# Kernel optimization log

Measured on AMD Instinct MI355X. Metric: run time of the kernel, lower is better.

The kernel has to match this reference:

```python
import jax, jax.numpy as jnp
import numpy as np

N_BUILD = 200000
N_COMM = 10000
E_BUILD = 1200000
E_COMM = 160000
D_B = 64    # building feature dim
D_C = 32    # community feature dim
H = 64      # hidden dim (comm embedding)
D_FUSE = D_B + H  # 128
N_CLS = 2


def gcn(x, src, dst, W, b):
    """PyG-style GCNConv with self-loops and symmetric normalization.
    out_i = sum_{j->i} h_j / sqrt(deg_j * deg_i) + h_i / deg_i + b, h = x @ W.
    deg counts in-edges plus the self-loop."""
    n = x.shape[0]
    h = x @ W                                   # [n, out]
    deg = jnp.ones((n,), x.dtype).at[dst].add(1.0)
    norm = jax.lax.rsqrt(deg)
    msg = h[src] * (norm[src] * norm[dst])[:, None]          # gather + edge weight
    agg = jax.ops.segment_sum(msg, dst, num_segments=n)      # scatter-add
    return agg + h * (1.0 / deg)[:, None] + b


def setup_inputs():
    key = jax.random.key(0)
    ks = jax.random.split(key, 24)
    f32 = jnp.float32

    def glorot(k, shape):
        scale = np.sqrt(2.0 / (shape[0] + shape[1])).astype(np.float32)
        return jax.random.normal(k, shape, dtype=f32) * scale

    inp = {
        "building_features": jax.random.normal(ks[0], (N_BUILD, D_B), dtype=f32),
        "community_features": jax.random.normal(ks[1], (N_COMM, D_C), dtype=f32),
        # GCN weights: comm 32->64->64, attention 128->2, building 128->128->64->2
        "W_c1": glorot(ks[2], (D_C, H)),   "b_c1": jnp.zeros((H,), f32),
        "W_c2": glorot(ks[3], (H, H)),     "b_c2": jnp.zeros((H,), f32),
        "W_att": glorot(ks[4], (D_FUSE, 2)), "b_att": jnp.zeros((2,), f32),
        "W_b1": glorot(ks[5], (D_FUSE, D_FUSE)), "b_b1": jnp.zeros((D_FUSE,), f32),
        "W_b2": glorot(ks[6], (D_FUSE, H)),       "b_b2": jnp.zeros((H,), f32),
        "W_b3": glorot(ks[7], (H, N_CLS)),         "b_b3": jnp.zeros((N_CLS,), f32),
        # edge lists (int) and index maps
        "b_src": jax.random.randint(ks[8], (E_BUILD,), 0, N_BUILD, dtype=jnp.int32),
        "b_dst": jax.random.randint(ks[9], (E_BUILD,), 0, N_BUILD, dtype=jnp.int32),
        "c_src": jax.random.randint(ks[10], (E_COMM,), 0, N_COMM, dtype=jnp.int32),
        "c_dst": jax.random.randint(ks[11], (E_COMM,), 0, N_COMM, dtype=jnp.int32),
        "building_to_comm_mapping": jax.random.randint(ks[12], (N_BUILD,), 0, N_COMM, dtype=jnp.int32),
        # Batch.from_data_list ordering: here identity permutation of buildings
        "local_to_global": jnp.arange(N_BUILD, dtype=jnp.int32),
    }
    return inp


def reference(building_features, community_features,
              W_c1, b_c1, W_c2, b_c2, W_att, b_att,
              W_b1, b_b1, W_b2, b_b2, W_b3, b_b3,
              b_src, b_dst, c_src, c_dst,
              building_to_comm_mapping, local_to_global):
    # Community GNN (dropout is identity in eval)
    comm_x = jax.nn.relu(gcn(community_features, c_src, c_dst, W_c1, b_c1))
    comm_x = jax.nn.relu(gcn(comm_x, c_src, c_dst, W_c2, b_c2))

    # Irregular gather: per-building community embedding
    building_comm = comm_x[building_to_comm_mapping]          # [N_build, H]

    # Feature attention: softmax gate over the two modalities
    logits = jnp.concatenate([building_features, building_comm], axis=1) @ W_att + b_att
    a = jax.nn.softmax(logits, axis=1)                        # [N_build, 2]
    fused = jnp.concatenate([building_features * a[:, 0:1],
                             building_comm * a[:, 1:2]], axis=1)  # [N_build, 128]

    # Batched building GNN over disjoint per-community subgraphs
    local_x = fused[local_to_global]
    x = jax.nn.relu(gcn(local_x, b_src, b_dst, W_b1, b_b1))
    x = jax.nn.relu(gcn(x, b_src, b_dst, W_b2, b_b2))
    x = gcn(x, b_src, b_dst, W_b3, b_b3)                      # [N_build, 2]

    # Scatter back to global order, then log-softmax
    combined = jnp.zeros((building_features.shape[0], N_CLS), x.dtype)
    combined = combined.at[local_to_global].set(x)
    return jax.nn.log_softmax(combined, axis=1)
```

## Files before the change

### kernel.cpp

```cpp
#include <hip/hip_runtime.h>
#include <hip/hip_bf16.h>
#include <math.h>

#define N_BUILD 200000
#define N_COMM  10000
#define E_BUILD 1200000
#define E_COMM  160000
#define NB_B 196
#define NB_C 10
#define CHUNK 2048
#define CB_B ((E_BUILD + CHUNK - 1) / CHUNK)
#define CB_C ((E_COMM  + CHUNK - 1) / CHUNK)

typedef __bf16 bf16x8 __attribute__((ext_vector_type(8)));
typedef float  f32x4  __attribute__((ext_vector_type(4)));

__device__ __forceinline__ unsigned short f2b(float f) {
    unsigned int u = __builtin_bit_cast(unsigned int, f);
    u += 0x7fffu + ((u >> 16) & 1u);
    return (unsigned short)(u >> 16);
}
__device__ __forceinline__ float b2f(unsigned short h) {
    unsigned int u = ((unsigned int)h) << 16;
    return __builtin_bit_cast(float, u);
}
__device__ __forceinline__ unsigned int pk2(float a, float b) {
    return (unsigned int)f2b(a) | ((unsigned int)f2b(b) << 16);
}
__device__ __forceinline__ void up8(uint4 v, float* r) {
    r[0] = b2f((unsigned short)v.x); r[1] = b2f((unsigned short)(v.x >> 16));
    r[2] = b2f((unsigned short)v.y); r[3] = b2f((unsigned short)(v.y >> 16));
    r[4] = b2f((unsigned short)v.z); r[5] = b2f((unsigned short)(v.z >> 16));
    r[6] = b2f((unsigned short)v.w); r[7] = b2f((unsigned short)(v.w >> 16));
}

#define INIT_TOT (N_BUILD + N_COMM + 2 * N_BUILD + N_COMM * 32 + 2048 + 4096 + 16384 + 8192)
__global__ __launch_bounds__(256) void init_k(int* cnt_b, int* cnt_c, float* out,
                                              const float* __restrict__ cF, unsigned short* __restrict__ cFb,
                                              const float* __restrict__ W_c1, unsigned short* __restrict__ Wt_c1,
                                              const float* __restrict__ W_c2, unsigned short* __restrict__ Wt_c2,
                                              const float* __restrict__ W_b1, unsigned short* __restrict__ Wt_b1,
                                              const float* __restrict__ W_b2, unsigned short* __restrict__ Wt_b2) {
    int i = blockIdx.x * blockDim.x + threadIdx.x;
    if (i < N_BUILD) { cnt_b[i] = 0; return; }
    i -= N_BUILD;
    if (i < N_COMM) { cnt_c[i] = 0; return; }
    i -= N_COMM;
    if (i < 2 * N_BUILD) { out[i] = -0.69314718056f; return; }
    i -= 2 * N_BUILD;
    if (i < N_COMM * 32) { cFb[i] = f2b(cF[i]); return; }
    i -= N_COMM * 32;
    if (i < 2048) { Wt_c1[(i % 64) * 32 + i / 64] = f2b(W_c1[i]); return; }
    i -= 2048;
    if (i < 4096) { Wt_c2[(i % 64) * 64 + i / 64] = f2b(W_c2[i]); return; }
    i -= 4096;
    if (i < 16384) { Wt_b1[(i % 128) * 128 + i / 128] = f2b(W_b1[i]); return; }
    i -= 16384;
    if (i < 8192) { Wt_b2[(i % 64) * 128 + i / 64] = f2b(W_b2[i]); }
}


__global__ __launch_bounds__(256) void hist2_k(int* cnt_b, const int* __restrict__ b_dst,
                                               int* cnt_c, const int* __restrict__ c_dst) {
    int i = blockIdx.x * blockDim.x + threadIdx.x;
    if (i < E_BUILD) atomicAdd(&cnt_b[b_dst[i]], 1);
    else if (i < E_BUILD + E_COMM) atomicAdd(&cnt_c[c_dst[i - E_BUILD]], 1);
}

__global__ __launch_bounds__(256) void scan1m_k(const int* __restrict__ cnt_b, int* __restrict__ ex_b, int* __restrict__ bs_b,
                                                const int* __restrict__ cnt_c, int* __restrict__ ex_c, int* __restrict__ bs_c) {
    __shared__ int sdata[256];
    const int tid = threadIdx.x;
    const int* cnt; int* ex; int* bs; int n, blk;
    if ((int)blockIdx.x < NB_B) { cnt = cnt_b; ex = ex_b; bs = bs_b; n = N_BUILD; blk = blockIdx.x; }
    else                        { cnt = cnt_c; ex = ex_c; bs = bs_c; n = N_COMM;  blk = blockIdx.x - NB_B; }
    const int base = blk * 1024 + tid * 4;
    int v[4]; int s = 0;
#pragma unroll
    for (int j = 0; j < 4; ++j) { v[j] = (base + j < n) ? cnt[base + j] : 0; s += v[j]; }
    sdata[tid] = s; __syncthreads();
    for (int off = 1; off < 256; off <<= 1) {
        int t = (tid >= off) ? sdata[tid - off] : 0;
        __syncthreads();
        sdata[tid] += t;
        __syncthreads();
    }
    if (tid == 255) bs[blk] = sdata[255];
    int run = sdata[tid] - s;
#pragma unroll
    for (int j = 0; j < 4; ++j) { if (base + j < n) ex[base + j] = run; run += v[j]; }
}

__global__ __launch_bounds__(256) void scan2m_k(int* bs_b, int* bs_c) {
    __shared__ int sdata[256];
    int* bs = (blockIdx.x == 0) ? bs_b : bs_c;
    int nb  = (blockIdx.x == 0) ? NB_B : NB_C;
    const int tid = threadIdx.x;
    int v = (tid < nb) ? bs[tid] : 0;
    sdata[tid] = v; __syncthreads();
    for (int off = 1; off < 256; off <<= 1) {
        int t = (tid >= off) ? sdata[tid - off] : 0;
        __syncthreads();
        sdata[tid] += t;
        __syncthreads();
    }
    if (tid < nb) bs[tid] = sdata[tid] - v;
}

__global__ __launch_bounds__(256) void finalizem_k(const int* __restrict__ cnt_b, int* rp_b, const int* __restrict__ bo_b,
                                                   int* cur_b, float* di_b,
                                                   const int* __restrict__ cnt_c, int* rp_c, const int* __restrict__ bo_c,
                                                   int* cur_c, float* di_c) {
    int i = blockIdx.x * blockDim.x + threadIdx.x;
    if (i < N_BUILD) {
        int cc = cnt_b[i];
        int r = rp_b[i] + bo_b[i >> 10];
        rp_b[i] = r; cur_b[i] = r; di_b[i] = 1.0f / (float)(cc + 1);
        if (i == 0) { rp_b[N_BUILD] = E_BUILD; rp_c[N_COMM] = E_COMM; }
    } else if (i < N_BUILD + N_COMM) {
        int ic = i - N_BUILD;
        int cc = cnt_c[ic];
        int r = rp_c[ic] + bo_c[ic >> 10];
        rp_c[ic] = r; cur_c[ic] = r; di_c[ic] = 1.0f / (float)(cc + 1);
    }
}

template<int NDIV>
__device__ __forceinline__ void scatter_part(const int* __restrict__ src, const int* __restrict__ dst,
                                             int* cur, const float* __restrict__ di,
                                             int2* __restrict__ cse, int E, int cid, int x) {
    int base = cid * CHUNK + threadIdx.x;
#pragma unroll
    for (int j = 0; j < CHUNK / 256; ++j, base += 256) {
        if (base < E) {
            int d = dst[base];
            if ((unsigned)d / (unsigned)NDIV == (unsigned)x) {
                int s = src[base];
                int pos = atomicAdd(&cur[d], 1);
                cse[pos] = make_int2(s, __float_as_int(sqrtf(di[s] * di[d])));
            }
        }
    }
}

__global__ __launch_bounds__(256) void csr_scatterp_k(const int* __restrict__ b_src, const int* __restrict__ b_dst,
                                                      int* cur_b, const float* __restrict__ di_b, int2* __restrict__ cse_b,
                                                      const int* __restrict__ c_src, const int* __restrict__ c_dst,
                                                      int* cur_c, const float* __restrict__ di_c, int2* __restrict__ cse_c) {
    int bid = blockIdx.x;
    if (bid < 8 * CB_B) {
        scatter_part<N_BUILD / 8>(b_src, b_dst, cur_b, di_b, cse_b, E_BUILD, bid >> 3, bid & 7);
    } else {
        bid -= 8 * CB_B;
        scatter_part<N_COMM / 8>(c_src, c_dst, cur_c, di_c, cse_c, E_COMM, bid >> 3, bid & 7);
    }
}

template<int K, int N, bool GUARD>
__global__ __launch_bounds__(256) void gemm_mfma_k(const unsigned short* __restrict__ X,
                                                   const unsigned short* __restrict__ Wt,
                                                   unsigned short* __restrict__ H, int M) {
    constexpr int GPR = K / 8;
    __shared__ unsigned short sA[64 * K];
    __shared__ unsigned short sB[N * K];
    const int tid  = threadIdx.x;
    const int row0 = blockIdx.x * 64;

    for (int idx = tid; idx < 64 * GPR; idx += 256) {
        int r = idx / GPR, g = idx % GPR;
        uint4 v = make_uint4(0u, 0u, 0u, 0u);
        if (!GUARD || row0 + r < M)
            v = *(const uint4*)&X[(size_t)(row0 + r) * K + g * 8];
        int gs = g ^ (r & (GPR - 1));
        *(uint4*)&sA[r * K + gs * 8] = v;
    }
    for (int idx = tid; idx < N * GPR; idx += 256) {
        int r = idx / GPR, g = idx % GPR;
        uint4 v = *(const uint4*)&Wt[(size_t)r * K + g * 8];
        int gs = g ^ (r & (GPR - 1));
        *(uint4*)&sB[r * K + gs * 8] = v;
    }
    __syncthreads();

    const int wave = tid >> 6, lane = tid & 63;
    const int rA = wave * 16 + (lane & 15);
    const int kg = lane >> 4;

    f32x4 zero = {0.f, 0.f, 0.f, 0.f};
    f32x4 acc[N / 16];
#pragma unroll
    for (int t = 0; t < N / 16; ++t) acc[t] = zero;

#pragma unroll
    for (int ks = 0; ks < K / 32; ++ks) {
        int gA = (ks * 4 + kg) ^ (rA & (GPR - 1));
        bf16x8 a = *(const bf16x8*)&sA[rA * K + gA * 8];
#pragma unroll
        for (int t = 0; t < N / 16; ++t) {
            int rB = t * 16 + (lane & 15);
            int gB = (ks * 4 + kg) ^ (rB & (GPR - 1));
            bf16x8 b = *(const bf16x8*)&sB[rB * K + gB * 8];
            acc[t] = __builtin_amdgcn_mfma_f32_16x16x32_bf16(a, b, acc[t], 0, 0, 0);
        }
    }

    const int crow = wave * 16 + (lane >> 4) * 4;
    const int ccol = lane & 15;
#pragma unroll
    for (int t = 0; t < N / 16; ++t) {
#pragma unroll
        for (int j = 0; j < 4; ++j) {
            int r = row0 + crow + j;
            if (!GUARD || r < M)
                H[(size_t)r * N + t * 16 + ccol] = f2b(acc[t][j]);
        }
    }
}

__global__ __launch_bounds__(256) void attscal_k(const float* __restrict__ bF,
                                                 const unsigned short* __restrict__ cx,
                                                 const int* __restrict__ map,
                                                 const int* __restrict__ l2g,
                                                 const float* __restrict__ Watt,
                                                 const float* __restrict__ batt,
                                                 unsigned short* __restrict__ bFl,
                                                 float2* __restrict__ afus,
                                                 int* __restrict__ mbl, int n) {
    __shared__ float sW0[128], sW1[128];
    if (threadIdx.x < 128) {
        sW0[threadIdx.x] = Watt[threadIdx.x * 2 + 0];
        sW1[threadIdx.x] = Watt[threadIdx.x * 2 + 1];
    }
    __syncthreads();
    int gid = blockIdx.x * blockDim.x + threadIdx.x;
    int i = gid >> 3, j = gid & 7;
    if (i >= n) return;
    int g = l2g[i];
    int mg = map[g];
    const float* f1 = &bF[(size_t)g * 64 + j * 8];
    const unsigned short* f2 = &cx[(size_t)mg * 64 + j * 8];
    float r1[8], r2[8];
    {
        float4 v0 = *(const float4*)&f1[0];
        float4 v1 = *(const float4*)&f1[4];
        r1[0]=v0.x; r1[1]=v0.y; r1[2]=v0.z; r1[3]=v0.w;
        r1[4]=v1.x; r1[5]=v1.y; r1[6]=v1.z; r1[7]=v1.w;
        uint4 u = *(const uint4*)&f2[0];
        up8(u, r2);
    }
    float l0 = 0.f, l1 = 0.f;
#pragma unroll
    for (int k = 0; k < 8; ++k) {
        l0 = fmaf(r1[k], sW0[j * 8 + k], l0);
        l1 = fmaf(r1[k], sW1[j * 8 + k], l1);
        l0 = fmaf(r2[k], sW0[64 + j * 8 + k], l0);
        l1 = fmaf(r2[k], sW1[64 + j * 8 + k], l1);
    }
#pragma unroll
    for (int m = 1; m < 8; m <<= 1) {
        l0 += __shfl_xor(l0, m, 8);
        l1 += __shfl_xor(l1, m, 8);
    }
    l0 += batt[0]; l1 += batt[1];
    float mm = fmaxf(l0, l1);
    float e0 = __expf(l0 - mm), e1 = __expf(l1 - mm);
    float inv = 1.0f / (e0 + e1);
    uint4 o;
    o.x = pk2(r1[0], r1[1]); o.y = pk2(r1[2], r1[3]);
    o.z = pk2(r1[4], r1[5]); o.w = pk2(r1[6], r1[7]);
    *(uint4*)&bFl[(size_t)i * 64 + j * 8] = o;
    if (j == 0) {
        afus[i] = make_float2(e0 * inv, e1 * inv);
        mbl[i] = mg;
    }
}

__global__ __launch_bounds__(256) void agg1_k(const int* __restrict__ rowptr,
                                              const int2* __restrict__ cse,
                                              const unsigned short* __restrict__ bFl,
                                              const unsigned short* __restrict__ cx2,
                                              const int* __restrict__ mbl,
                                              const float2* __restrict__ afus,
                                              const float* __restrict__ dinv,
                                              unsigned short* __restrict__ y1,
                                              int nGrp) {
    int wid = (blockIdx.x * blockDim.x + threadIdx.x) >> 6;
    int lane = threadIdx.x & 63;
    if (wid >= nGrp) return;
    int node = wid * 4 + (lane >> 4);
    int sl = lane & 15;
    bool upper = sl >= 8;
    int c = (sl & 7) * 8;
    int beg = rowptr[node], end = rowptr[node + 1];
    float2 afi = afus[node];
    int mbi = mbl[node];
    uint4 hv = upper ? *(const uint4*)&cx2[(size_t)mbi * 64 + c]
                     : *(const uint4*)&bFl[(size_t)node * 64 + c];
    float selfw = dinv[node] * (upper ? afi.y : afi.x);
    float acc[8];
#pragma unroll
    for (int i = 0; i < 8; ++i) acc[i] = 0.f;
    for (int p = beg; p < end; p += 8) {
        int2 q[8];
#pragma unroll
        for (int t = 0; t < 8; ++t) { int e = p + t; q[t] = cse[e < end ? e : 0]; }
        float2 af[8]; int mb[8];
#pragma unroll
        for (int t = 0; t < 8; ++t) { af[t] = afus[q[t].x]; mb[t] = mbl[q[t].x]; }
        uint4 v[8];
#pragma unroll
        for (int t = 0; t < 8; ++t) {
            const unsigned short* base = upper ? &cx2[(size_t)mb[t] * 64 + c]
                                               : &bFl[(size_t)q[t].x * 64 + c];
            v[t] = *(const uint4*)base;
        }
#pragma unroll
        for (int t = 0; t < 8; ++t) {
            float w = (p + t < end) ? __int_as_float(q[t].y) : 0.f;
            float wa = w * (upper ? af[t].y : af[t].x);
            float r[8]; up8(v[t], r);
#pragma unroll
            for (int i = 0; i < 8; ++i) acc[i] = fmaf(r[i], wa, acc[i]);
        }
    }
    float hr[8]; up8(hv, hr);
#pragma unroll
    for (int i = 0; i < 8; ++i) acc[i] = fmaf(hr[i], selfw, acc[i]);
    uint4 ov;
    ov.x = pk2(acc[0], acc[1]); ov.y = pk2(acc[2], acc[3]);
    ov.z = pk2(acc[4], acc[5]); ov.w = pk2(acc[6], acc[7]);
    *(uint4*)&y1[(size_t)node * 128 + sl * 8] = ov;
}

__global__ __launch_bounds__(256) void gemm2x_k(const unsigned short* __restrict__ y1,
                                                const unsigned short* __restrict__ Wt1,
                                                const float* __restrict__ b1,
                                                const unsigned short* __restrict__ Wt2,
                                                unsigned short* __restrict__ H) {
    constexpr int K = 128, GPR = 16;
    __shared__ unsigned short sA[64 * K];
    __shared__ unsigned short sB1[128 * K];
    __shared__ unsigned short sB2[64 * K];
    const int tid = threadIdx.x;
    const int row0 = blockIdx.x * 64;
    for (int idx = tid; idx < 64 * GPR; idx += 256) {
        int r = idx / GPR, g = idx % GPR;
        uint4 v = *(const uint4*)&y1[(size_t)(row0 + r) * K + g * 8];
        int gs = g ^ (r & (GPR - 1));
        *(uint4*)&sA[r * K + gs * 8] = v;
    }
    for (int idx = tid; idx < 128 * GPR; idx += 256) {
        int r = idx / GPR, g = idx % GPR;
        uint4 v = *(const uint4*)&Wt1[(size_t)r * K + g * 8];
        int gs = g ^ (r & (GPR - 1));
        *(uint4*)&sB1[r * K + gs * 8] = v;
    }
    for (int idx = tid; idx < 64 * GPR; idx += 256) {
        int r = idx / GPR, g = idx % GPR;
        uint4 v = *(const uint4*)&Wt2[(size_t)r * K + g * 8];
        int gs = g ^ (r & (GPR - 1));
        *(uint4*)&sB2[r * K + gs * 8] = v;
    }
    __syncthreads();
    const int wave = tid >> 6, lane = tid & 63;
    const int rA = wave * 16 + (lane & 15);
    const int kg = lane >> 4;
    const int crow = wave * 16 + (lane >> 4) * 4;
    const int ccol = lane & 15;
    f32x4 zero = {0.f, 0.f, 0.f, 0.f};
    f32x4 acc1[8];
#pragma unroll
    for (int t = 0; t < 8; ++t) acc1[t] = zero;
#pragma unroll
    for (int ks = 0; ks < 4; ++ks) {
        int gA = (ks * 4 + kg) ^ (rA & (GPR - 1));
        bf16x8 a = *(const bf16x8*)&sA[rA * K + gA * 8];
#pragma unroll
        for (int t = 0; t < 8; ++t) {
            int rB = t * 16 + (lane & 15);
            int gB = (ks * 4 + kg) ^ (rB & (GPR - 1));
            bf16x8 b = *(const bf16x8*)&sB1[rB * K + gB * 8];
            acc1[t] = __builtin_amdgcn_mfma_f32_16x16x32_bf16(a, b, acc1[t], 0, 0, 0);
        }
    }
    __syncthreads();
#pragma unroll
    for (int t = 0; t < 8; ++t) {
        float bv = b1[t * 16 + ccol];
#pragma unroll
        for (int j = 0; j < 4; ++j) {
            float x = fmaxf(acc1[t][j] + bv, 0.f);
            int r = crow + j;
            int ch = t * 16 + ccol;
            sA[r * K + (((ch >> 3) ^ (r & (GPR - 1))) << 3) + (ch & 7)] = f2b(x);
        }
    }
    __syncthreads();
    f32x4 acc2[4];
#pragma unroll
    for (int t = 0; t < 4; ++t) acc2[t] = zero;
#pragma unroll
    for (int ks = 0; ks < 4; ++ks) {
        int gA = (ks * 4 + kg) ^ (rA & (GPR - 1));
        bf16x8 a = *(const bf16x8*)&sA[rA * K + gA * 8];
#pragma unroll
        for (int t = 0; t < 4; ++t) {
            int rB = t * 16 + (lane & 15);
            int gB = (ks * 4 + kg) ^ (rB & (GPR - 1));
            bf16x8 b = *(const bf16x8*)&sB2[rB * K + gB * 8];
            acc2[t] = __builtin_amdgcn_mfma_f32_16x16x32_bf16(a, b, acc2[t], 0, 0, 0);
        }
    }
#pragma unroll
    for (int t = 0; t < 4; ++t)
#pragma unroll
        for (int jj = 0; jj < 4; ++jj)
            H[(size_t)(row0 + crow + jj) * 64 + t * 16 + ccol] = f2b(acc2[t][jj]);
}

template<int F, bool RELU>
__global__ __launch_bounds__(256) void gatherF_k(const int* __restrict__ rowptr,
                                                 const int2* __restrict__ cse,
                                                 const unsigned short* __restrict__ h,
                                                 const float* __restrict__ dinv,
                                                 const float* __restrict__ bias,
                                                 unsigned short* __restrict__ out, int nGrp) {
    constexpr int LPN = F / 8;
    constexpr int NPW = 64 / LPN;
    int wid = (blockIdx.x * blockDim.x + threadIdx.x) >> 6;
    int lane = threadIdx.x & 63;
    if (wid >= nGrp) return;
    int node = wid * NPW + lane / LPN;
    int c = (lane % LPN) * 8;
    int beg = rowptr[node], end = rowptr[node + 1];
    uint4 hv = *(const uint4*)&h[(size_t)node * F + c];
    float iv = dinv[node];
    float4 bb0 = *(const float4*)&bias[c];
    float4 bb1 = *(const float4*)&bias[c + 4];
    float acc[8];
#pragma unroll
    for (int i = 0; i < 8; ++i) acc[i] = 0.f;
    for (int p = beg; p < end; p += 8) {
        int2 q[8]; uint4 v[8];
#pragma unroll
        for (int t = 0; t < 8; ++t) { int e = p + t; q[t] = cse[e < end ? e : 0]; }
#pragma unroll
        for (int t = 0; t < 8; ++t) v[t] = *(const uint4*)&h[(size_t)q[t].x * F + c];
#pragma unroll
        for (int t = 0; t < 8; ++t) {
            float w = (p + t < end) ? __int_as_float(q[t].y) : 0.f;
            float r[8]; up8(v[t], r);
#pragma unroll
            for (int i = 0; i < 8; ++i) acc[i] = fmaf(r[i], w, acc[i]);
        }
    }
    float hr[8]; up8(hv, hr);
    float o[8];
    o[0] = fmaf(hr[0], iv, acc[0]) + bb0.x; o[1] = fmaf(hr[1], iv, acc[1]) + bb0.y;
    o[2] = fmaf(hr[2], iv, acc[2]) + bb0.z; o[3] = fmaf(hr[3], iv, acc[3]) + bb0.w;
    o[4] = fmaf(hr[4], iv, acc[4]) + bb1.x; o[5] = fmaf(hr[5], iv, acc[5]) + bb1.y;
    o[6] = fmaf(hr[6], iv, acc[6]) + bb1.z; o[7] = fmaf(hr[7], iv, acc[7]) + bb1.w;
    if (RELU) {
#pragma unroll
        for (int i = 0; i < 8; ++i) o[i] = fmaxf(o[i], 0.f);
    }
    uint4 ov;
    ov.x = pk2(o[0], o[1]); ov.y = pk2(o[2], o[3]);
    ov.z = pk2(o[4], o[5]); ov.w = pk2(o[6], o[7]);
    *(uint4*)&out[(size_t)node * F + c] = ov;
}

__global__ __launch_bounds__(256) void gather64_dot_k(const int* __restrict__ rowptr,
                                                      const int2* __restrict__ cse,
                                                      const unsigned short* __restrict__ h,
                                                      const float* __restrict__ dinv,
                                                      const float* __restrict__ bias,
                                                      const float* __restrict__ W3,
                                                      float* __restrict__ Dh, int nOct) {
    int wid = (blockIdx.x * blockDim.x + threadIdx.x) >> 6;
    int lane = threadIdx.x & 63;
    if (wid >= nOct) return;
    int node = wid * 8 + (lane >> 3);
    int sl = lane & 7, c = sl * 8;
    int beg = rowptr[node], end = rowptr[node + 1];
    uint4 hv = *(const uint4*)&h[(size_t)node * 64 + c];
    float iv = dinv[node];
    float4 bb0 = *(const float4*)&bias[c];
    float4 bb1 = *(const float4*)&bias[c + 4];
    float4 w4[4];
#pragma unroll
    for (int i = 0; i < 4; ++i) w4[i] = *(const float4*)&W3[c * 2 + i * 4];
    float acc[8];
#pragma unroll
    for (int i = 0; i < 8; ++i) acc[i] = 0.f;
    for (int p = beg; p < end; p += 8) {
        int2 q[8]; uint4 v[8];
#pragma unroll
        for (int t = 0; t < 8; ++t) { int e = p + t; q[t] = cse[e < end ? e : 0]; }
#pragma unroll
        for (int t = 0; t < 8; ++t) v[t] = *(const uint4*)&h[(size_t)q[t].x * 64 + c];
#pragma unroll
        for (int t = 0; t < 8; ++t) {
            float w = (p + t < end) ? __int_as_float(q[t].y) : 0.f;
            float r[8]; up8(v[t], r);
#pragma unroll
            for (int i = 0; i < 8; ++i) acc[i] = fmaf(r[i], w, acc[i]);
        }
    }
    float hr[8]; up8(hv, hr);
    float o[8];
    o[0] = fmaf(hr[0], iv, acc[0]) + bb0.x; o[1] = fmaf(hr[1], iv, acc[1]) + bb0.y;
    o[2] = fmaf(hr[2], iv, acc[2]) + bb0.z; o[3] = fmaf(hr[3], iv, acc[3]) + bb0.w;
    o[4] = fmaf(hr[4], iv, acc[4]) + bb1.x; o[5] = fmaf(hr[5], iv, acc[5]) + bb1.y;
    o[6] = fmaf(hr[6], iv, acc[6]) + bb1.z; o[7] = fmaf(hr[7], iv, acc[7]) + bb1.w;
#pragma unroll
    for (int i = 0; i < 8; ++i) o[i] = fmaxf(o[i], 0.f);
    float d0 = 0.f, d1 = 0.f;
#pragma unroll
    for (int i = 0; i < 4; ++i) {
        d0 = fmaf(o[2*i],   w4[i].x, d0); d0 = fmaf(o[2*i+1], w4[i].z, d0);
        d1 = fmaf(o[2*i],   w4[i].y, d1); d1 = fmaf(o[2*i+1], w4[i].w, d1);
    }
#pragma unroll
    for (int m = 1; m < 8; m <<= 1) {
        d0 += __shfl_xor(d0, m, 8);
        d1 += __shfl_xor(d1, m, 8);
    }
    if (sl == 0) {
        Dh[2 * (size_t)node + 0] = d0;
        Dh[2 * (size_t)node + 1] = d1;
    }
}

__global__ __launch_bounds__(256) void gather2_logsm_k(const int* __restrict__ rowptr,
                                                       const int2* __restrict__ cse,
                                                       const float* __restrict__ h2,
                                                       const float* __restrict__ dinv,
                                                       const float* __restrict__ bias,
                                                       const int* __restrict__ l2g,
                                                       float* __restrict__ out, int n) {
    int i = blockIdx.x * blockDim.x + threadIdx.x;
    if (i >= n) return;
    int beg = rowptr[i], end = rowptr[i + 1];
    float2 hv = *(const float2*)&h2[2 * (size_t)i];
    float iv = dinv[i];
    float a = 0.f, b = 0.f;
    for (int p = beg; p < end; p += 8) {
        int2 q[8]; float2 v[8];
#pragma unroll
        for (int t = 0; t < 8; ++t) { int e = p + t; q[t] = cse[e < end ? e : 0]; }
#pragma unroll
        for (int t = 0; t < 8; ++t) v[t] = *(const float2*)&h2[2 * (size_t)q[t].x];
#pragma unroll
        for (int t = 0; t < 8; ++t) {
            float w = (p + t < end) ? __int_as_float(q[t].y) : 0.f;
            a = fmaf(v[t].x, w, a);
            b = fmaf(v[t].y, w, b);
        }
    }
    a = fmaf(hv.x, iv, a) + bias[0];
    b = fmaf(hv.y, iv, b) + bias[1];
    float m = fmaxf(a, b);
    float ls = m + logf(__expf(a - m) + __expf(b - m));
    int g = l2g[i];
    out[2 * (size_t)g + 0] = a - ls;
    out[2 * (size_t)g + 1] = b - ls;
}


static inline dim3 g1(long long n, int tpb = 256) { return dim3((unsigned)((n + tpb - 1) / tpb)); }

extern "C" void kernel_launch(void* const* d_in, const int* in_sizes, int n_in,
                              void* d_out, int out_size, void* d_ws, size_t ws_size,
                              hipStream_t stream) {
    const float* bF   = (const float*)d_in[0];
    const float* cF   = (const float*)d_in[1];
    const float* W_c1 = (const float*)d_in[2];
    const float* b_c1 = (const float*)d_in[3];
    const float* W_c2 = (const float*)d_in[4];
    const float* b_c2 = (const float*)d_in[5];
    const float* W_at = (const float*)d_in[6];
    const float* b_at = (const float*)d_in[7];
    const float* W_b1 = (const float*)d_in[8];
    const float* b_b1 = (const float*)d_in[9];
    const float* W_b2 = (const float*)d_in[10];
    const float* b_b2 = (const float*)d_in[11];
    const float* W_b3 = (const float*)d_in[12];
    const float* b_b3 = (const float*)d_in[13];
    const int* b_src = (const int*)d_in[14];
    const int* b_dst = (const int*)d_in[15];
    const int* c_src = (const int*)d_in[16];
    const int* c_dst = (const int*)d_in[17];
    const int* map   = (const int*)d_in[18];
    const int* l2g   = (const int*)d_in[19];
    float* out = (float*)d_out;

    char* p = (char*)d_ws;
    auto alloc = [&](size_t bytes) { char* q = p; p += (bytes + 15) & ~(size_t)15; return q; };
    int*   cnt_b    = (int*)  alloc(N_BUILD * 4);
    int*   rowptr_b = (int*)  alloc((N_BUILD + 4) * 4);
    int*   cursor_b = (int*)  alloc(N_BUILD * 4);
    int*   bsum_b   = (int*)  alloc(256 * 4);
    int*   cnt_c    = (int*)  alloc(N_COMM * 4);
    int*   rowptr_c = (int*)  alloc((N_COMM + 4) * 4);
    int*   cursor_c = (int*)  alloc(N_COMM * 4);
    int*   bsum_c   = (int*)  alloc(256 * 4);
    int2*  cse_b    = (int2*) alloc((size_t)E_BUILD * 8);
    int2*  cse_c    = (int2*) alloc((size_t)E_COMM * 8);
    float* dinv_b   = (float*)alloc(N_BUILD * 4);
    float* dinv_c   = (float*)alloc(N_COMM * 4);
    unsigned short* cFb    = (unsigned short*)alloc((size_t)N_COMM * 32 * 2);
    unsigned short* Wt_c1  = (unsigned short*)alloc(64 * 32 * 2);
    unsigned short* Wt_c2  = (unsigned short*)alloc(64 * 64 * 2);
    unsigned short* Wt_b1  = (unsigned short*)alloc(128 * 128 * 2);
    unsigned short* Wt_b2  = (unsigned short*)alloc(64 * 128 * 2);
    unsigned short* ch_bf  = (unsigned short*)alloc((size_t)N_COMM * 64 * 2);
    unsigned short* cx1_bf = (unsigned short*)alloc((size_t)N_COMM * 64 * 2);
    unsigned short* cx2_bf = (unsigned short*)alloc((size_t)N_COMM * 64 * 2);
    unsigned short* bFl    = (unsigned short*)alloc((size_t)N_BUILD * 64 * 2);
    float2* afus           = (float2*)        alloc((size_t)N_BUILD * 8);
    int*    mbl            = (int*)           alloc((size_t)N_BUILD * 4);
    unsigned short* y1_bf  = (unsigned short*)alloc((size_t)N_BUILD * 128 * 2);
    unsigned short* h2_bf  = (unsigned short*)alloc((size_t)N_BUILD * 64 * 2);
    float* Dh = (float*)alloc((size_t)N_BUILD * 2 * 4);

    init_k<<<g1(INIT_TOT), 256, 0, stream>>>(cnt_b, cnt_c, out,
                                             cF, cFb, W_c1, Wt_c1, W_c2, Wt_c2, W_b1, Wt_b1, W_b2, Wt_b2);
    hist2_k<<<g1(E_BUILD + E_COMM), 256, 0, stream>>>(cnt_b, b_dst, cnt_c, c_dst);
    scan1m_k<<<NB_B + NB_C, 256, 0, stream>>>(cnt_b, rowptr_b, bsum_b, cnt_c, rowptr_c, bsum_c);
    scan2m_k<<<2, 256, 0, stream>>>(bsum_b, bsum_c);
    finalizem_k<<<g1(N_BUILD + N_COMM), 256, 0, stream>>>(cnt_b, rowptr_b, bsum_b, cursor_b, dinv_b,
                                                          cnt_c, rowptr_c, bsum_c, cursor_c, dinv_c);
    csr_scatterp_k<<<8 * (CB_B + CB_C), 256, 0, stream>>>(b_src, b_dst, cursor_b, dinv_b, cse_b,
                                                          c_src, c_dst, cursor_c, dinv_c, cse_c);

    gemm_mfma_k<32, 64, true><<<dim3((N_COMM + 63) / 64), 256, 0, stream>>>(cFb, Wt_c1, ch_bf, N_COMM);
    gatherF_k<64, true><<<g1((long long)(N_COMM / 8) * 64), 256, 0, stream>>>(rowptr_c, cse_c, ch_bf, dinv_c, b_c1, cx1_bf, N_COMM / 8);

    gemm_mfma_k<64, 64, true><<<dim3((N_COMM + 63) / 64), 256, 0, stream>>>(cx1_bf, Wt_c2, ch_bf, N_COMM);
    gatherF_k<64, true><<<g1((long long)(N_COMM / 8) * 64), 256, 0, stream>>>(rowptr_c, cse_c, ch_bf, dinv_c, b_c2, cx2_bf, N_COMM / 8);

    attscal_k<<<g1((long long)N_BUILD * 8), 256, 0, stream>>>(bF, cx2_bf, map, l2g, W_at, b_at,
                                                              bFl, afus, mbl, N_BUILD);

    agg1_k<<<g1((long long)(N_BUILD / 4) * 64), 256, 0, stream>>>(rowptr_b, cse_b, bFl, cx2_bf, mbl, afus,
                                                                  dinv_b, y1_bf, N_BUILD / 4);

    gemm2x_k<<<dim3(N_BUILD / 64), 256, 0, stream>>>(y1_bf, Wt_b1, b_b1, Wt_b2, h2_bf);

    gather64_dot_k<<<g1((long long)(N_BUILD / 8) * 64), 256, 0, stream>>>(rowptr_b, cse_b, h2_bf, dinv_b, b_b2, W_b3, Dh, N_BUILD / 8);

    gather2_logsm_k<<<g1(N_BUILD), 256, 0, stream>>>(rowptr_b, cse_b, Dh, dinv_b, b_b3, l2g, out, N_BUILD);
}
```

Measured before the change: 356.3 us.

## Precompute attention-scaled edge weights and community ids into CSR edge arrays

Splits the CSR scatter into separate community and building kernels, and moves the building scatter after the attention kernel. The building scatter can then store a second per-edge array holding the edge weight times the source's community attention, together with the source's community id. The attention kernel now pre-scales building features by the first attention weight and packs dinv, the second attention weight and the community index into one int4 per node. In agg1, this removes the per-neighbour afus and mbl gathers (dependent random loads), at the cost of an extra 8-byte-per-edge array, random nmeta reads during the scatter, and one more kernel launch.

```diff
diff --git a/kernel.cpp b/kernel.cpp
--- a/kernel.cpp
+++ b/kernel.cpp
@@ -125,34 +125,44 @@
     }
 }
 
-template<int NDIV>
-__device__ __forceinline__ void scatter_part(const int* __restrict__ src, const int* __restrict__ dst,
-                                             int* cur, const float* __restrict__ di,
-                                             int2* __restrict__ cse, int E, int cid, int x) {
+__global__ __launch_bounds__(256) void csr_scatterc_k(const int* __restrict__ c_src, const int* __restrict__ c_dst,
+                                                      int* cur_c, const float* __restrict__ di_c, int2* __restrict__ cse_c) {
+    const int cid = blockIdx.x >> 3, x = blockIdx.x & 7;
+    constexpr int NDIV = N_COMM / 8;
     int base = cid * CHUNK + threadIdx.x;
 #pragma unroll
     for (int j = 0; j < CHUNK / 256; ++j, base += 256) {
-        if (base < E) {
-            int d = dst[base];
+        if (base < E_COMM) {
+            int d = c_dst[base];
             if ((unsigned)d / (unsigned)NDIV == (unsigned)x) {
-                int s = src[base];
-                int pos = atomicAdd(&cur[d], 1);
-                cse[pos] = make_int2(s, __float_as_int(sqrtf(di[s] * di[d])));
+                int s = c_src[base];
+                int pos = atomicAdd(&cur_c[d], 1);
+                cse_c[pos] = make_int2(s, __float_as_int(sqrtf(di_c[s] * di_c[d])));
             }
         }
     }
 }
 
-__global__ __launch_bounds__(256) void csr_scatterp_k(const int* __restrict__ b_src, const int* __restrict__ b_dst,
-                                                      int* cur_b, const float* __restrict__ di_b, int2* __restrict__ cse_b,
-                                                      const int* __restrict__ c_src, const int* __restrict__ c_dst,
-                                                      int* cur_c, const float* __restrict__ di_c, int2* __restrict__ cse_c) {
-    int bid = blockIdx.x;
-    if (bid < 8 * CB_B) {
-        scatter_part<N_BUILD / 8>(b_src, b_dst, cur_b, di_b, cse_b, E_BUILD, bid >> 3, bid & 7);
-    } else {
-        bid -= 8 * CB_B;
-        scatter_part<N_COMM / 8>(c_src, c_dst, cur_c, di_c, cse_c, E_COMM, bid >> 3, bid & 7);
+__global__ __launch_bounds__(256) void csr_scatterb_k(const int* __restrict__ b_src, const int* __restrict__ b_dst,
+                                                      int* cur_b, const float* __restrict__ di_b,
+                                                      const int4* __restrict__ nmeta,
+                                                      int2* __restrict__ cse_b, int2* __restrict__ exb) {
+    const int cid = blockIdx.x >> 3, x = blockIdx.x & 7;
+    constexpr int NDIV = N_BUILD / 8;
+    int base = cid * CHUNK + threadIdx.x;
+#pragma unroll
+    for (int j = 0; j < CHUNK / 256; ++j, base += 256) {
+        if (base < E_BUILD) {
+            int d = b_dst[base];
+            if ((unsigned)d / (unsigned)NDIV == (unsigned)x) {
+                int s = b_src[base];
+                int pos = atomicAdd(&cur_b[d], 1);
+                int4 nm = nmeta[s];
+                float w = sqrtf(__int_as_float(nm.x) * di_b[d]);
+                cse_b[pos] = make_int2(s, __float_as_int(w));
+                exb[pos]   = make_int2(__float_as_int(w * __int_as_float(nm.y)), nm.z);
+            }
+        }
     }
 }
 
@@ -223,9 +233,9 @@
                                                  const int* __restrict__ l2g,
                                                  const float* __restrict__ Watt,
                                                  const float* __restrict__ batt,
+                                                 const float* __restrict__ dinv,
                                                  unsigned short* __restrict__ bFl,
-                                                 float2* __restrict__ afus,
-                                                 int* __restrict__ mbl, int n) {
+                                                 int4* __restrict__ nmeta, int n) {
     __shared__ float sW0[128], sW1[128];
     if (threadIdx.x < 128) {
         sW0[threadIdx.x] = Watt[threadIdx.x * 2 + 0];
@@ -265,23 +275,21 @@
     float mm = fmaxf(l0, l1);
     float e0 = __expf(l0 - mm), e1 = __expf(l1 - mm);
     float inv = 1.0f / (e0 + e1);
+    float a0 = e0 * inv, a1 = e1 * inv;
     uint4 o;
-    o.x = pk2(r1[0], r1[1]); o.y = pk2(r1[2], r1[3]);
-    o.z = pk2(r1[4], r1[5]); o.w = pk2(r1[6], r1[7]);
+    o.x = pk2(r1[0]*a0, r1[1]*a0); o.y = pk2(r1[2]*a0, r1[3]*a0);
+    o.z = pk2(r1[4]*a0, r1[5]*a0); o.w = pk2(r1[6]*a0, r1[7]*a0);
     *(uint4*)&bFl[(size_t)i * 64 + j * 8] = o;
-    if (j == 0) {
-        afus[i] = make_float2(e0 * inv, e1 * inv);
-        mbl[i] = mg;
-    }
+    if (j == 0)
+        nmeta[i] = make_int4(__float_as_int(dinv[i]), __float_as_int(a1), mg, 0);
 }
 
 __global__ __launch_bounds__(256) void agg1_k(const int* __restrict__ rowptr,
                                               const int2* __restrict__ cse,
+                                              const int2* __restrict__ exb,
                                               const unsigned short* __restrict__ bFl,
                                               const unsigned short* __restrict__ cx2,
-                                              const int* __restrict__ mbl,
-                                              const float2* __restrict__ afus,
-                                              const float* __restrict__ dinv,
+                                              const int4* __restrict__ nmeta,
                                               unsigned short* __restrict__ y1,
                                               int nGrp) {
     int wid = (blockIdx.x * blockDim.x + threadIdx.x) >> 6;
@@ -292,35 +300,33 @@
     bool upper = sl >= 8;
     int c = (sl & 7) * 8;
     int beg = rowptr[node], end = rowptr[node + 1];
-    float2 afi = afus[node];
-    int mbi = mbl[node];
-    uint4 hv = upper ? *(const uint4*)&cx2[(size_t)mbi * 64 + c]
+    int4 nm = nmeta[node];
+    float di = __int_as_float(nm.x);
+    uint4 hv = upper ? *(const uint4*)&cx2[(size_t)nm.z * 64 + c]
                      : *(const uint4*)&bFl[(size_t)node * 64 + c];
-    float selfw = dinv[node] * (upper ? afi.y : afi.x);
+    float selfw = upper ? di * __int_as_float(nm.y) : di;
+    const int2* es = upper ? exb : cse;
     float acc[8];
 #pragma unroll
     for (int i = 0; i < 8; ++i) acc[i] = 0.f;
     for (int p = beg; p < end; p += 8) {
         int2 q[8];
 #pragma unroll
-        for (int t = 0; t < 8; ++t) { int e = p + t; q[t] = cse[e < end ? e : 0]; }
-        float2 af[8]; int mb[8];
-#pragma unroll
-        for (int t = 0; t < 8; ++t) { af[t] = afus[q[t].x]; mb[t] = mbl[q[t].x]; }
+        for (int t = 0; t < 8; ++t) { int e = p + t; q[t] = es[e < end ? e : 0]; }
         uint4 v[8];
 #pragma unroll
         for (int t = 0; t < 8; ++t) {
-            const unsigned short* base = upper ? &cx2[(size_t)mb[t] * 64 + c]
+            const unsigned short* base = upper ? &cx2[(size_t)q[t].y * 64 + c]
                                                : &bFl[(size_t)q[t].x * 64 + c];
             v[t] = *(const uint4*)base;
         }
 #pragma unroll
         for (int t = 0; t < 8; ++t) {
-            float w = (p + t < end) ? __int_as_float(q[t].y) : 0.f;
-            float wa = w * (upper ? af[t].y : af[t].x);
+            float sc = __int_as_float(upper ? q[t].x : q[t].y);
+            float w = (p + t < end) ? sc : 0.f;
             float r[8]; up8(v[t], r);
 #pragma unroll
-            for (int i = 0; i < 8; ++i) acc[i] = fmaf(r[i], wa, acc[i]);
+            for (int i = 0; i < 8; ++i) acc[i] = fmaf(r[i], w, acc[i]);
         }
     }
     float hr[8]; up8(hv, hr);
@@ -606,6 +612,7 @@
     int*   cursor_c = (int*)  alloc(N_COMM * 4);
     int*   bsum_c   = (int*)  alloc(256 * 4);
     int2*  cse_b    = (int2*) alloc((size_t)E_BUILD * 8);
+    int2*  exb      = (int2*) alloc((size_t)E_BUILD * 8);
     int2*  cse_c    = (int2*) alloc((size_t)E_COMM * 8);
     float* dinv_b   = (float*)alloc(N_BUILD * 4);
     float* dinv_c   = (float*)alloc(N_COMM * 4);
@@ -618,8 +625,7 @@
     unsigned short* cx1_bf = (unsigned short*)alloc((size_t)N_COMM * 64 * 2);
     unsigned short* cx2_bf = (unsigned short*)alloc((size_t)N_COMM * 64 * 2);
     unsigned short* bFl    = (unsigned short*)alloc((size_t)N_BUILD * 64 * 2);
-    float2* afus           = (float2*)        alloc((size_t)N_BUILD * 8);
-    int*    mbl            = (int*)           alloc((size_t)N_BUILD * 4);
+    int4*  nmeta           = (int4*)          alloc((size_t)N_BUILD * 16);
     unsigned short* y1_bf  = (unsigned short*)alloc((size_t)N_BUILD * 128 * 2);
     unsigned short* h2_bf  = (unsigned short*)alloc((size_t)N_BUILD * 64 * 2);
     float* Dh = (float*)alloc((size_t)N_BUILD * 2 * 4);
@@ -631,20 +637,20 @@
     scan2m_k<<<2, 256, 0, stream>>>(bsum_b, bsum_c);
     finalizem_k<<<g1(N_BUILD + N_COMM), 256, 0, stream>>>(cnt_b, rowptr_b, bsum_b, cursor_b, dinv_b,
                                                           cnt_c, rowptr_c, bsum_c, cursor_c, dinv_c);
-    csr_scatterp_k<<<8 * (CB_B + CB_C), 256, 0, stream>>>(b_src, b_dst, cursor_b, dinv_b, cse_b,
-                                                          c_src, c_dst, cursor_c, dinv_c, cse_c);
+    csr_scatterc_k<<<8 * CB_C, 256, 0, stream>>>(c_src, c_dst, cursor_c, dinv_c, cse_c);
 
     gemm_mfma_k<32, 64, true><<<dim3((N_COMM + 63) / 64), 256, 0, stream>>>(cFb, Wt_c1, ch_bf, N_COMM);
     gatherF_k<64, true><<<g1((long long)(N_COMM / 8) * 64), 256, 0, stream>>>(rowptr_c, cse_c, ch_bf, dinv_c, b_c1, cx1_bf, N_COMM / 8);
-
     gemm_mfma_k<64, 64, true><<<dim3((N_COMM + 63) / 64), 256, 0, stream>>>(cx1_bf, Wt_c2, ch_bf, N_COMM);
     gatherF_k<64, true><<<g1((long long)(N_COMM / 8) * 64), 256, 0, stream>>>(rowptr_c, cse_c, ch_bf, dinv_c, b_c2, cx2_bf, N_COMM / 8);
 
     attscal_k<<<g1((long long)N_BUILD * 8), 256, 0, stream>>>(bF, cx2_bf, map, l2g, W_at, b_at,
-                                                              bFl, afus, mbl, N_BUILD);
-
-    agg1_k<<<g1((long long)(N_BUILD / 4) * 64), 256, 0, stream>>>(rowptr_b, cse_b, bFl, cx2_bf, mbl, afus,
-                                                                  dinv_b, y1_bf, N_BUILD / 4);
+                                                              dinv_b, bFl, nmeta, N_BUILD);
+
+    csr_scatterb_k<<<8 * CB_B, 256, 0, stream>>>(b_src, b_dst, cursor_b, dinv_b, nmeta, cse_b, exb);
+
+    agg1_k<<<g1((long long)(N_BUILD / 4) * 64), 256, 0, stream>>>(rowptr_b, cse_b, exb, bFl, cx2_bf,
+                                                                  nmeta, y1_bf, N_BUILD / 4);
 
     gemm2x_k<<<dim3(N_BUILD / 64), 256, 0, stream>>>(y1_bf, Wt_b1, b_b1, Wt_b2, h2_bf);
 
```

Result: no change. 351.2 us (-1.4%).
